# Performance work log

Hardware: AMD Instinct MI355X
Metric: run time of the kernel (lower is better)

Reference implementation:

```python
import jax, jax.numpy as jnp
import numpy as np

D = 512       # d_model
H = 8         # n_heads
HD = D // H   # head_dim = 64
BS = 64       # block_size
B = 1
S = 8192
NB = S // BS  # 128 blocks
THRESH = 0.3


def setup_inputs() -> dict:
    key = jax.random.key(0)
    ks = jax.random.split(key, 6)
    sc = 0.02
    return {
        "x": jax.random.normal(ks[0], (B, S, D), jnp.float32),
        "w_qkv": (jax.random.normal(ks[1], (D, 3 * D)) * sc).astype(jnp.float32),
        "b_qkv": jnp.zeros((3 * D,), jnp.float32),
        "w_out": (jax.random.normal(ks[2], (D, D)) * sc).astype(jnp.float32),
        "b_out": jnp.zeros((D,), jnp.float32),
        "w_r1": (jax.random.normal(ks[3], (D, 128)) * sc).astype(jnp.float32),
        "b_r1": jnp.zeros((128,), jnp.float32),
        "w_r2": (jax.random.normal(ks[4], (128, 1)) * sc).astype(jnp.float32),
        "b_r2": jnp.full((1,), 0.5, jnp.float32),  # sigmoid(~0.5)>0.3 -> non-degenerate mask
    }


def reference(x, w_qkv, b_qkv, w_out, b_out, w_r1, b_r1, w_r2, b_r2):
    Bx, Sx, Dx = x.shape
    qkv = (x @ w_qkv + b_qkv).reshape(Bx, Sx, 3, H, HD)
    q = jnp.transpose(qkv[:, :, 0], (0, 2, 1, 3))  # [B,H,S,HD]
    k = jnp.transpose(qkv[:, :, 1], (0, 2, 1, 3))
    v = jnp.transpose(qkv[:, :, 2], (0, 2, 1, 3))

    # --- router: per-block importance from mean-pooled q block (d_model features) ---
    qb = q.reshape(Bx, H, NB, BS, HD)
    rep = jnp.transpose(qb.mean(axis=3), (0, 2, 1, 3)).reshape(Bx, NB, Dx)  # [B,NB,D]
    imp = jax.nn.sigmoid(jax.nn.relu(rep @ w_r1 + b_r1) @ w_r2 + b_r2)[..., 0]  # [B,NB]
    keep = (imp.mean(axis=0) >= THRESH).astype(x.dtype)  # [NB], shared across batch (torch uses batch-mean)

    kb = k.reshape(Bx, H, NB, BS, HD)
    vb = v.reshape(Bx, H, NB, BS, HD)
    tri = jnp.triu(jnp.ones((BS, BS), bool), 1)  # strict upper triangle within diagonal block
    jidx = jnp.arange(NB)
    scale = 1.0 / np.sqrt(HD)

    def step(carry, i):
        q_i = jax.lax.dynamic_slice_in_dim(q, i * BS, BS, axis=2)        # [B,H,BSq,HD]
        s = jnp.einsum('bhqd,bhjkd->bhqjk', q_i, kb) * scale             # [B,H,BSq,NB,BSk]
        causal = (jidx == i)[None, :, None] & tri[:, None, :]            # [BSq,NB,BSk]
        s = jnp.where(causal[None, None], -jnp.inf, s)
        p = jax.nn.softmax(s, axis=-1)                                   # softmax PER key-block (as in torch loop)
        wj = keep * keep[i]                                              # block pair gate [NB]
        o = jnp.einsum('bhqjk,j,bhjkd->bhqd', p, wj, vb)                 # sum of gated per-block contributions
        return carry, o

    _, outs = jax.lax.scan(step, None, jnp.arange(NB))                   # [NB,B,H,BSq,HD]
    attn = jnp.transpose(outs, (1, 2, 0, 3, 4)).reshape(Bx, H, Sx, HD)
    attn = jnp.transpose(attn, (0, 2, 1, 3)).reshape(Bx, Sx, Dx)
    return attn @ w_out + b_out
```

## Files before the change

### kernel.cpp

```cpp
#include <hip/hip_runtime.h>

typedef unsigned short u16;
typedef unsigned int u32;
typedef __attribute__((ext_vector_type(8))) short short8;
typedef __attribute__((ext_vector_type(4))) short short4v;
typedef __attribute__((ext_vector_type(4))) float f32x4;
typedef __attribute__((ext_vector_type(4))) float float4v;
typedef __attribute__((ext_vector_type(2))) u32 u32x2;
typedef __attribute__((ext_vector_type(4))) u32 u32x4;

#define S_LEN 8192
#define NHEAD 8
#define NBLK  128
#define SCALE_C 0.18033688011112042f

#if __has_builtin(__builtin_amdgcn_permlane16_swap) && __has_builtin(__builtin_amdgcn_permlane32_swap)
#define HAVE_PLSWAP 1
#else
#define HAVE_PLSWAP 0
#endif

__device__ __forceinline__ u16 f2b(float f) {
    union { float f; unsigned u; } v; v.f = f;
    unsigned r = v.u + 0x7FFFu + ((v.u >> 16) & 1u);
    return (u16)(r >> 16);
}
__device__ __forceinline__ float b2f(u16 b) {
    union { float f; unsigned u; } v; v.u = ((unsigned)b) << 16; return v.f;
}
__device__ __forceinline__ u32 cvt_pk_bf16(float lo, float hi) {
    u32 r;
    asm("v_cvt_pk_bf16_f32 %0, %1, %2" : "=v"(r) : "v"(lo), "v"(hi));
    return r;
}
#if HAVE_PLSWAP
__device__ __forceinline__ void pl16swap(u32& a, u32& b) {
    u32x2 r = __builtin_amdgcn_permlane16_swap(a, b, false, false);
    a = r[0]; b = r[1];
}
__device__ __forceinline__ void pl32swap(u32& a, u32& b) {
    u32x2 r = __builtin_amdgcn_permlane32_swap(a, b, false, false);
    a = r[0]; b = r[1];
}
#endif
__device__ __forceinline__ int swz(int row, int colByte) {
    return row * 128 + (colByte ^ ((row & 7) << 4));
}

__global__ __launch_bounds__(256) void cvt_x_kernel(const float* __restrict__ x, u16* __restrict__ xb) {
    int idx = blockIdx.x * 256 + threadIdx.x;
    float4v v = *((const float4v*)x + idx);
    short4v o;
    #pragma unroll
    for (int r = 0; r < 4; ++r) o[r] = (short)f2b(v[r]);
    *((short4v*)xb + idx) = o;
}

__global__ __launch_bounds__(256) void cvt_T_kernel(const float* __restrict__ w, u16* __restrict__ wt, int C) {
    int idx = blockIdx.x * 256 + threadIdx.x;
    int r = idx & 511, cc = idx >> 9;
    wt[idx] = f2b(w[(size_t)r * C + cc]);
}

__device__ __forceinline__ void gemm128_core(const u16* __restrict__ A,
                                             const u16* __restrict__ Bt,
                                             int m0, int n0, char* As, char* Bs,
                                             f32x4 acc[4][4]) {
    const int tid = threadIdx.x;
    const int lane = tid & 63, wid = tid >> 6;
    const int q16 = lane >> 4, l16 = lane & 15;
    const int wm = wid >> 1, wn = wid & 1;
    #pragma unroll 1
    for (int kt = 0; kt < 8; ++kt) {
        const int k0 = kt * 64;
        short8 ra[4], rb[4];
        #pragma unroll
        for (int p = 0; p < 4; ++p) {
            int c = tid + p * 256;
            int row = c >> 3, col = c & 7;
            ra[p] = *(const short8*)(A  + (size_t)(m0 + row) * 512 + k0 + col * 8);
            rb[p] = *(const short8*)(Bt + (size_t)(n0 + row) * 512 + k0 + col * 8);
        }
        __syncthreads();
        #pragma unroll
        for (int p = 0; p < 4; ++p) {
            int c = tid + p * 256;
            int row = c >> 3, col = c & 7;
            *(short8*)(As + swz(row, col * 16)) = ra[p];
            *(short8*)(Bs + swz(row, col * 16)) = rb[p];
        }
        __syncthreads();
        #pragma unroll
        for (int kk = 0; kk < 2; ++kk) {
            short8 a[4], b[4];
            #pragma unroll
            for (int t = 0; t < 4; ++t) {
                int arow = wm * 64 + t * 16 + l16;
                a[t] = *(const short8*)(As + swz(arow, (kk * 32 + q16 * 8) * 2));
                int brow = wn * 64 + t * 16 + l16;
                b[t] = *(const short8*)(Bs + swz(brow, (kk * 32 + q16 * 8) * 2));
            }
            #pragma unroll
            for (int mt = 0; mt < 4; ++mt)
                #pragma unroll
                for (int nt = 0; nt < 4; ++nt)
                    acc[mt][nt] = __builtin_amdgcn_mfma_f32_16x16x32_bf16(a[mt], b[nt], acc[mt][nt], 0, 0, 0);
        }
    }
}

__global__ __launch_bounds__(256) void qkv_gemm(const u16* __restrict__ xb, const u16* __restrict__ wqkvT,
                                                const float* __restrict__ bqkv,
                                                u16* __restrict__ qb, u16* __restrict__ kb, u16* __restrict__ vt) {
    __shared__ char smem[32768];
    f32x4 acc[4][4];
    #pragma unroll
    for (int a = 0; a < 4; ++a)
        #pragma unroll
        for (int b = 0; b < 4; ++b) acc[a][b] = (f32x4){0.f, 0.f, 0.f, 0.f};
    const int m0 = blockIdx.x * 128, n0 = blockIdx.y * 128;
    gemm128_core(xb, wqkvT, m0, n0, smem, smem + 16384, acc);

    const int lane = threadIdx.x & 63, wid = threadIdx.x >> 6;
    const int q16 = lane >> 4, l16 = lane & 15;
    const int wm = wid >> 1, wn = wid & 1;
    #pragma unroll
    for (int mt = 0; mt < 4; ++mt) {
        #pragma unroll
        for (int nt = 0; nt < 4; ++nt) {
            int n = n0 + wn * 64 + nt * 16 + l16;
            float bias = bqkv[n];
            int t = n >> 9, h = (n >> 6) & 7, d = n & 63;
            int sb = m0 + wm * 64 + mt * 16 + q16 * 4;
            f32x4 v = acc[mt][nt];
            if (t == 2) {
                short4v pk;
                #pragma unroll
                for (int r = 0; r < 4; ++r) pk[r] = (short)f2b(v[r] + bias);
                *(short4v*)(vt + (size_t)(h * 64 + d) * S_LEN + sb) = pk;
            } else {
                u16* dst = (t == 0) ? qb : kb;
                float scale = (t == 0) ? SCALE_C : 1.0f;
                #pragma unroll
                for (int r = 0; r < 4; ++r)
                    dst[(size_t)(h * S_LEN + sb + r) * 64 + d] = f2b((v[r] + bias) * scale);
            }
        }
    }
}

__global__ __launch_bounds__(256) void out_gemm(const u16* __restrict__ a0, const u16* __restrict__ a1,
                                                const u16* __restrict__ wotT,
                                                const float* __restrict__ bout, float* __restrict__ out) {
    __shared__ char smem[32768];
    f32x4 acc[4][4];
    #pragma unroll
    for (int a = 0; a < 4; ++a)
        #pragma unroll
        for (int b = 0; b < 4; ++b) acc[a][b] = (f32x4){0.f, 0.f, 0.f, 0.f};
    const int m0 = blockIdx.x * 128, n0 = blockIdx.y * 128;
    gemm128_core(a0, wotT, m0, n0, smem, smem + 16384, acc);
    gemm128_core(a1, wotT, m0, n0, smem, smem + 16384, acc);

    const int lane = threadIdx.x & 63, wid = threadIdx.x >> 6;
    const int q16 = lane >> 4, l16 = lane & 15;
    const int wm = wid >> 1, wn = wid & 1;
    #pragma unroll
    for (int mt = 0; mt < 4; ++mt) {
        #pragma unroll
        for (int nt = 0; nt < 4; ++nt) {
            int n = n0 + wn * 64 + nt * 16 + l16;
            float bias = bout[n];
            int sb = m0 + wm * 64 + mt * 16 + q16 * 4;
            #pragma unroll
            for (int r = 0; r < 4; ++r)
                out[(size_t)(sb + r) * 512 + n] = acc[mt][nt][r] + bias;
        }
    }
}

__global__ __launch_bounds__(256) void router_kernel(const u16* __restrict__ qb,
                                                     const float* __restrict__ w_r1, const float* __restrict__ b_r1,
                                                     const float* __restrict__ w_r2, const float* __restrict__ b_r2,
                                                     float* __restrict__ keepf) {
    const int nb = blockIdx.x, tid = threadIdx.x;
    __shared__ float rep[512];
    __shared__ float h1[128];
    for (int dim = tid; dim < 512; dim += 256) {
        int h = dim >> 6, d = dim & 63;
        const u16* p = qb + (size_t)(h * S_LEN + nb * 64) * 64 + d;
        float s = 0.f;
        #pragma unroll 4
        for (int t = 0; t < 64; ++t) s += b2f(p[t * 64]);
        rep[dim] = s * (0.015625f / SCALE_C);
    }
    __syncthreads();
    if (tid < 128) {
        float a = b_r1[tid];
        for (int k = 0; k < 512; ++k) a += rep[k] * w_r1[k * 128 + tid];
        h1[tid] = fmaxf(a, 0.f);
    }
    __syncthreads();
    if (tid < 64) {
        float v = h1[tid] * w_r2[tid] + h1[tid + 64] * w_r2[tid + 64];
        #pragma unroll
        for (int off = 32; off; off >>= 1) v += __shfl_down(v, off);
        if (tid == 0) {
            float z = v + b_r2[0];
            keepf[nb] = (z >= -0.84729786f) ? 1.0f : 0.0f;
        }
    }
}

__global__ __launch_bounds__(256) void attn_kernel(const u16* __restrict__ qb, const u16* __restrict__ kb,
                                                   const u16* __restrict__ vt, const float* __restrict__ keepf,
                                                   u16* __restrict__ att0, u16* __restrict__ att1) {
    const int i = blockIdx.x, h = blockIdx.y, jh = blockIdx.z;
    const int j0 = jh * 64;
    u16* __restrict__ att = jh ? att1 : att0;
    const int tid = threadIdx.x, lane = tid & 63, wid = tid >> 6;
    const int q16 = lane >> 4, l16 = lane & 15;
    __shared__ char smem[32768];

    short8 bq0, bq1;
    {
        const u16* qrow = qb + (size_t)(h * S_LEN + i * 64 + wid * 16 + l16) * 64;
        bq0 = *(const short8*)(qrow + q16 * 8);
        bq1 = *(const short8*)(qrow + 32 + q16 * 8);
    }
    const float keep_i = keepf[i];
    const int qloc = wid * 16 + l16;

    f32x4 o[4];
    #pragma unroll
    for (int t = 0; t < 4; ++t) o[t] = (f32x4){0.f, 0.f, 0.f, 0.f};

    const int r0 = tid >> 3, col = tid & 7;
    const u16* kptr = kb + (size_t)(h * S_LEN + j0 * 64 + r0) * 64 + col * 8;
    const u16* vptr = vt + (size_t)(h * 64 + r0) * S_LEN + j0 * 64 + col * 8;
    const int swa = swz(r0, col * 16), swb = swz(r0 + 32, col * 16);
#if !HAVE_PLSWAP
    const bool sel_hi = (q16 >= 2);
    const int idx0 = (((2 * q16 + 0) & 3) * 16 + l16) * 4;
    const int idx1 = (((2 * q16 + 1) & 3) * 16 + l16) * 4;
#endif

    short8 kr0 = *(const short8*)kptr;
    short8 kr1 = *(const short8*)(kptr + 2048);
    short8 vr0 = *(const short8*)vptr;
    short8 vr1 = *(const short8*)(vptr + (size_t)32 * S_LEN);
    *(short8*)(smem + swa) = kr0;
    *(short8*)(smem + swb) = kr1;
    *(short8*)(smem + 8192 + swa) = vr0;
    *(short8*)(smem + 8192 + swb) = vr1;
    kr0 = *(const short8*)(kptr + 4096);
    kr1 = *(const short8*)(kptr + 4096 + 2048);
    vr0 = *(const short8*)(vptr + 64);
    vr1 = *(const short8*)(vptr + (size_t)32 * S_LEN + 64);
    __syncthreads();

    for (int jj = 0; jj < 64; ++jj) {
        char* Kc = smem + ((jj & 1) << 14);
        char* Vc = Kc + 8192;
        char* Kn = smem + (((jj + 1) & 1) << 14);
        char* Vn = Kn + 8192;
        if (jj < 63) {
            *(short8*)(Kn + swa) = kr0;
            *(short8*)(Kn + swb) = kr1;
            *(short8*)(Vn + swa) = vr0;
            *(short8*)(Vn + swb) = vr1;
        }
        if (jj < 62) {
            const u16* kn = kptr + (size_t)(jj + 2) * 4096;
            const u16* vn = vptr + (size_t)(jj + 2) * 64;
            kr0 = *(const short8*)kn;
            kr1 = *(const short8*)(kn + 2048);
            vr0 = *(const short8*)vn;
            vr1 = *(const short8*)(vn + (size_t)32 * S_LEN);
        }
        const float g = keep_i * keepf[j0 + jj];

        f32x4 s4[4];
        __builtin_amdgcn_s_setprio(1);
        #pragma unroll
        for (int n0 = 0; n0 < 4; ++n0) {
            short8 ka0 = *(const short8*)(Kc + swz(n0 * 16 + l16, q16 * 16));
            short8 ka1 = *(const short8*)(Kc + swz(n0 * 16 + l16, 64 + q16 * 16));
            f32x4 a = (f32x4){0.f, 0.f, 0.f, 0.f};
            a = __builtin_amdgcn_mfma_f32_16x16x32_bf16(ka0, bq0, a, 0, 0, 0);
            a = __builtin_amdgcn_mfma_f32_16x16x32_bf16(ka1, bq1, a, 0, 0, 0);
            s4[n0] = a;
        }
        __builtin_amdgcn_s_setprio(0);

        float pv[4][4];
        #pragma unroll
        for (int n0 = 0; n0 < 4; ++n0)
            #pragma unroll
            for (int r = 0; r < 4; ++r)
                pv[n0][r] = __builtin_amdgcn_exp2f(s4[n0][r]);
        if (j0 + jj == i) {
            #pragma unroll
            for (int n0 = 0; n0 < 4; ++n0)
                #pragma unroll
                for (int r = 0; r < 4; ++r)
                    if (n0 * 16 + q16 * 4 + r > qloc) pv[n0][r] = 0.f;
        }
        float sum = 0.f;
        #pragma unroll
        for (int n0 = 0; n0 < 4; ++n0)
            sum += (pv[n0][0] + pv[n0][1]) + (pv[n0][2] + pv[n0][3]);
#if HAVE_PLSWAP
        {
            u32 sa = __builtin_bit_cast(u32, sum), sb = sa;
            pl16swap(sa, sb);
            sum = __builtin_bit_cast(float, sa) + __builtin_bit_cast(float, sb);
            u32 sc = __builtin_bit_cast(u32, sum), sd = sc;
            pl32swap(sc, sd);
            sum = __builtin_bit_cast(float, sc) + __builtin_bit_cast(float, sd);
        }
#else
        sum += __shfl_xor(sum, 16);
        sum += __shfl_xor(sum, 32);
#endif
        const float rinv = g * __builtin_amdgcn_rcpf(sum);

        u32 dw[4][2];
        #pragma unroll
        for (int n0 = 0; n0 < 4; ++n0) {
            dw[n0][0] = cvt_pk_bf16(pv[n0][0] * rinv, pv[n0][1] * rinv);
            dw[n0][1] = cvt_pk_bf16(pv[n0][2] * rinv, pv[n0][3] * rinv);
        }
        short8 pb[2];
#if HAVE_PLSWAP
        #pragma unroll
        for (int kk = 0; kk < 2; ++kk) {
            u32 a0 = dw[2 * kk][0], b0 = dw[2 * kk + 1][0];
            pl32swap(a0, b0);
            pl16swap(a0, b0);
            u32 a1 = dw[2 * kk][1], b1 = dw[2 * kk + 1][1];
            pl32swap(a1, b1);
            pl16swap(a1, b1);
            u32x4 wv;
            wv[0] = a0; wv[1] = a1; wv[2] = b0; wv[3] = b1;
            pb[kk] = __builtin_bit_cast(short8, wv);
        }
#else
        {
            u32 pl0[4][2], pl1[4][2];
            #pragma unroll
            for (int n0 = 0; n0 < 4; ++n0)
                #pragma unroll
                for (int p = 0; p < 2; ++p) {
                    pl0[n0][p] = (u32)__builtin_amdgcn_ds_bpermute(idx0, (int)dw[n0][p]);
                    pl1[n0][p] = (u32)__builtin_amdgcn_ds_bpermute(idx1, (int)dw[n0][p]);
                }
            u32x4 bfa, bfb;
            bfa[0] = sel_hi ? pl0[1][0] : pl0[0][0];
            bfa[1] = sel_hi ? pl1[1][0] : pl1[0][0];
            bfa[2] = sel_hi ? pl0[1][1] : pl0[0][1];
            bfa[3] = sel_hi ? pl1[1][1] : pl1[0][1];
            bfb[0] = sel_hi ? pl0[3][0] : pl0[2][0];
            bfb[1] = sel_hi ? pl1[3][0] : pl1[2][0];
            bfb[2] = sel_hi ? pl0[3][1] : pl0[2][1];
            bfb[3] = sel_hi ? pl1[3][1] : pl1[2][1];
            pb[0] = __builtin_bit_cast(short8, bfa);
            pb[1] = __builtin_bit_cast(short8, bfb);
        }
#endif

        __builtin_amdgcn_s_setprio(1);
        #pragma unroll
        for (int dt = 0; dt < 4; ++dt) {
            short8 va0 = *(const short8*)(Vc + swz(dt * 16 + l16, q16 * 16));
            short8 va1 = *(const short8*)(Vc + swz(dt * 16 + l16, 64 + q16 * 16));
            o[dt] = __builtin_amdgcn_mfma_f32_16x16x32_bf16(va0, pb[0], o[dt], 0, 0, 0);
            o[dt] = __builtin_amdgcn_mfma_f32_16x16x32_bf16(va1, pb[1], o[dt], 0, 0, 0);
        }
        __builtin_amdgcn_s_setprio(0);

        __syncthreads();
    }

    u16* obase = att + (size_t)(i * 64 + wid * 16 + l16) * 512 + h * 64 + q16 * 4;
    #pragma unroll
    for (int dt = 0; dt < 4; ++dt) {
        u32x2 st;
        st[0] = cvt_pk_bf16(o[dt][0], o[dt][1]);
        st[1] = cvt_pk_bf16(o[dt][2], o[dt][3]);
        *(u32x2*)(obase + dt * 16) = st;
    }
}

static const size_t OFF_XB    = 0;
static const size_t OFF_WQKVT = OFF_XB    + (8u << 20);
static const size_t OFF_WOTT  = OFF_WQKVT + (2u << 20);
static const size_t OFF_QB    = OFF_WOTT  + (1u << 20);
static const size_t OFF_KB    = OFF_QB    + (8u << 20);
static const size_t OFF_VT    = OFF_KB    + (8u << 20);
static const size_t OFF_ATT   = OFF_VT    + (8u << 20);
static const size_t OFF_KEEP  = OFF_ATT   + (8u << 20);

extern "C" void kernel_launch(void* const* d_in, const int* in_sizes, int n_in,
                              void* d_out, int out_size, void* d_ws, size_t ws_size,
                              hipStream_t stream) {
    const float* x     = (const float*)d_in[0];
    const float* w_qkv = (const float*)d_in[1];
    const float* b_qkv = (const float*)d_in[2];
    const float* w_out = (const float*)d_in[3];
    const float* b_out = (const float*)d_in[4];
    const float* w_r1  = (const float*)d_in[5];
    const float* b_r1  = (const float*)d_in[6];
    const float* w_r2  = (const float*)d_in[7];
    const float* b_r2  = (const float*)d_in[8];
    float* out = (float*)d_out;
    char* ws = (char*)d_ws;
    u16* xb     = (u16*)(ws + OFF_XB);
    u16* wqkvT  = (u16*)(ws + OFF_WQKVT);
    u16* wotT   = (u16*)(ws + OFF_WOTT);
    u16* qb     = (u16*)(ws + OFF_QB);
    u16* kb     = (u16*)(ws + OFF_KB);
    u16* vt     = (u16*)(ws + OFF_VT);
    u16* attnb  = (u16*)(ws + OFF_ATT);
    u16* att1   = (u16*)(ws + OFF_XB);
    float* keepf = (float*)(ws + OFF_KEEP);

    cvt_x_kernel<<<4096, 256, 0, stream>>>(x, xb);
    cvt_T_kernel<<<3072, 256, 0, stream>>>(w_qkv, wqkvT, 1536);
    cvt_T_kernel<<<1024, 256, 0, stream>>>(w_out, wotT, 512);
    qkv_gemm<<<dim3(64, 12), 256, 0, stream>>>(xb, wqkvT, b_qkv, qb, kb, vt);
    router_kernel<<<128, 256, 0, stream>>>(qb, w_r1, b_r1, w_r2, b_r2, keepf);
    attn_kernel<<<dim3(128, 8, 2), 256, 0, stream>>>(qb, kb, vt, keepf, attnb, att1);
    out_gemm<<<dim3(64, 4), 256, 0, stream>>>(attnb, att1, wotT, b_out, out);
}
```

Before: 275.8 us.

## Double query rows per attention block and stage K/V via direct global-to-LDS loads

```diff
diff --git a/kernel.cpp b/kernel.cpp
--- a/kernel.cpp
+++ b/kernel.cpp
@@ -14,12 +14,6 @@
 #define NBLK  128
 #define SCALE_C 0.18033688011112042f
 
-#if __has_builtin(__builtin_amdgcn_permlane16_swap) && __has_builtin(__builtin_amdgcn_permlane32_swap)
-#define HAVE_PLSWAP 1
-#else
-#define HAVE_PLSWAP 0
-#endif
-
 __device__ __forceinline__ u16 f2b(float f) {
     union { float f; unsigned u; } v; v.f = f;
     unsigned r = v.u + 0x7FFFu + ((v.u >> 16) & 1u);
@@ -33,7 +27,6 @@
     asm("v_cvt_pk_bf16_f32 %0, %1, %2" : "=v"(r) : "v"(lo), "v"(hi));
     return r;
 }
-#if HAVE_PLSWAP
 __device__ __forceinline__ void pl16swap(u32& a, u32& b) {
     u32x2 r = __builtin_amdgcn_permlane16_swap(a, b, false, false);
     a = r[0]; b = r[1];
@@ -42,9 +35,13 @@
     u32x2 r = __builtin_amdgcn_permlane32_swap(a, b, false, false);
     a = r[0]; b = r[1];
 }
-#endif
 __device__ __forceinline__ int swz(int row, int colByte) {
     return row * 128 + (colByte ^ ((row & 7) << 4));
+}
+__device__ __forceinline__ void gload_lds(const void* g, void* l) {
+    __builtin_amdgcn_global_load_lds(
+        (const __attribute__((address_space(1))) void*)g,
+        (__attribute__((address_space(3))) void*)l, 16, 0, 0);
 }
 
 __global__ __launch_bounds__(256) void cvt_x_kernel(const float* __restrict__ x, u16* __restrict__ xb) {
@@ -73,21 +70,15 @@
     #pragma unroll 1
     for (int kt = 0; kt < 8; ++kt) {
         const int k0 = kt * 64;
-        short8 ra[4], rb[4];
+        __syncthreads();
         #pragma unroll
         for (int p = 0; p < 4; ++p) {
             int c = tid + p * 256;
-            int row = c >> 3, col = c & 7;
-            ra[p] = *(const short8*)(A  + (size_t)(m0 + row) * 512 + k0 + col * 8);
-            rb[p] = *(const short8*)(Bt + (size_t)(n0 + row) * 512 + k0 + col * 8);
-        }
-        __syncthreads();
-        #pragma unroll
-        for (int p = 0; p < 4; ++p) {
-            int c = tid + p * 256;
-            int row = c >> 3, col = c & 7;
-            *(short8*)(As + swz(row, col * 16)) = ra[p];
-            *(short8*)(Bs + swz(row, col * 16)) = rb[p];
+            int row = c >> 3, colp = (c & 7) ^ (row & 7);
+            char* dst = (char*)0 + (wid * 64 + p * 256) * 16;
+            gload_lds(A  + (size_t)(m0 + row) * 512 + k0 + colp * 8, As + (size_t)(wid * 64 + p * 256) * 16);
+            gload_lds(Bt + (size_t)(n0 + row) * 512 + k0 + colp * 8, Bs + (size_t)(wid * 64 + p * 256) * 16);
+            (void)dst;
         }
         __syncthreads();
         #pragma unroll
@@ -96,9 +87,9 @@
             #pragma unroll
             for (int t = 0; t < 4; ++t) {
                 int arow = wm * 64 + t * 16 + l16;
-                a[t] = *(const short8*)(As + swz(arow, (kk * 32 + q16 * 8) * 2));
+                a[t] = *(const short8*)(As + swz(arow, kk * 64 + q16 * 16));
                 int brow = wn * 64 + t * 16 + l16;
-                b[t] = *(const short8*)(Bs + swz(brow, (kk * 32 + q16 * 8) * 2));
+                b[t] = *(const short8*)(Bs + swz(brow, kk * 64 + q16 * 16));
             }
             #pragma unroll
             for (int mt = 0; mt < 4; ++mt)
@@ -212,9 +203,9 @@
     }
 }
 
-__global__ __launch_bounds__(256) void attn_kernel(const u16* __restrict__ qb, const u16* __restrict__ kb,
-                                                   const u16* __restrict__ vt, const float* __restrict__ keepf,
-                                                   u16* __restrict__ att0, u16* __restrict__ att1) {
+__global__ __launch_bounds__(256, 4) void attn_kernel(const u16* __restrict__ qb, const u16* __restrict__ kb,
+                                                      const u16* __restrict__ vt, const float* __restrict__ keepf,
+                                                      u16* __restrict__ att0, u16* __restrict__ att1) {
     const int i = blockIdx.x, h = blockIdx.y, jh = blockIdx.z;
     const int j0 = jh * 64;
     u16* __restrict__ att = jh ? att1 : att0;
@@ -222,173 +213,143 @@
     const int q16 = lane >> 4, l16 = lane & 15;
     __shared__ char smem[32768];
 
-    short8 bq0, bq1;
+    short8 bq[2][2];
+    #pragma unroll
+    for (int qh = 0; qh < 2; ++qh) {
+        const u16* qrow = qb + (size_t)(h * S_LEN + i * 128 + wid * 32 + qh * 16 + l16) * 64;
+        bq[qh][0] = *(const short8*)(qrow + q16 * 8);
+        bq[qh][1] = *(const short8*)(qrow + 32 + q16 * 8);
+    }
+    const int kq = i * 2 + (wid >> 1);
+    const float keep_i = keepf[kq];
+    const int qloc = (wid & 1) * 32 + l16;
+
+    f32x4 o[2][4];
+    #pragma unroll
+    for (int qh = 0; qh < 2; ++qh)
+        #pragma unroll
+        for (int t = 0; t < 4; ++t) o[qh][t] = (f32x4){0.f, 0.f, 0.f, 0.f};
+
+    const int rA = tid >> 3,          cA = (tid & 7) ^ (rA & 7);
+    const int rB = (tid + 256) >> 3,  cB = (tid & 7) ^ (rB & 7);
+    const u16* kb_h = kb + (size_t)h * S_LEN * 64;
+    const u16* vt_h = vt + (size_t)h * 64 * S_LEN;
+    const int ldw0 = wid * 1024, ldw1 = wid * 1024 + 4096;
+
     {
-        const u16* qrow = qb + (size_t)(h * S_LEN + i * 64 + wid * 16 + l16) * 64;
-        bq0 = *(const short8*)(qrow + q16 * 8);
-        bq1 = *(const short8*)(qrow + 32 + q16 * 8);
-    }
-    const float keep_i = keepf[i];
-    const int qloc = wid * 16 + l16;
-
-    f32x4 o[4];
-    #pragma unroll
-    for (int t = 0; t < 4; ++t) o[t] = (f32x4){0.f, 0.f, 0.f, 0.f};
-
-    const int r0 = tid >> 3, col = tid & 7;
-    const u16* kptr = kb + (size_t)(h * S_LEN + j0 * 64 + r0) * 64 + col * 8;
-    const u16* vptr = vt + (size_t)(h * 64 + r0) * S_LEN + j0 * 64 + col * 8;
-    const int swa = swz(r0, col * 16), swb = swz(r0 + 32, col * 16);
-#if !HAVE_PLSWAP
-    const bool sel_hi = (q16 >= 2);
-    const int idx0 = (((2 * q16 + 0) & 3) * 16 + l16) * 4;
-    const int idx1 = (((2 * q16 + 1) & 3) * 16 + l16) * 4;
-#endif
-
-    short8 kr0 = *(const short8*)kptr;
-    short8 kr1 = *(const short8*)(kptr + 2048);
-    short8 vr0 = *(const short8*)vptr;
-    short8 vr1 = *(const short8*)(vptr + (size_t)32 * S_LEN);
-    *(short8*)(smem + swa) = kr0;
-    *(short8*)(smem + swb) = kr1;
-    *(short8*)(smem + 8192 + swa) = vr0;
-    *(short8*)(smem + 8192 + swb) = vr1;
-    kr0 = *(const short8*)(kptr + 4096);
-    kr1 = *(const short8*)(kptr + 4096 + 2048);
-    vr0 = *(const short8*)(vptr + 64);
-    vr1 = *(const short8*)(vptr + (size_t)32 * S_LEN + 64);
+        char* base = smem;
+        gload_lds(kb_h + (size_t)(j0 * 64 + rA) * 64 + cA * 8, base + ldw0);
+        gload_lds(kb_h + (size_t)(j0 * 64 + rB) * 64 + cB * 8, base + ldw1);
+        gload_lds(vt_h + (size_t)rA * S_LEN + j0 * 64 + cA * 8, base + 8192 + ldw0);
+        gload_lds(vt_h + (size_t)rB * S_LEN + j0 * 64 + cB * 8, base + 8192 + ldw1);
+    }
     __syncthreads();
 
     for (int jj = 0; jj < 64; ++jj) {
+        const int j = j0 + jj;
         char* Kc = smem + ((jj & 1) << 14);
         char* Vc = Kc + 8192;
-        char* Kn = smem + (((jj + 1) & 1) << 14);
-        char* Vn = Kn + 8192;
         if (jj < 63) {
-            *(short8*)(Kn + swa) = kr0;
-            *(short8*)(Kn + swb) = kr1;
-            *(short8*)(Vn + swa) = vr0;
-            *(short8*)(Vn + swb) = vr1;
-        }
-        if (jj < 62) {
-            const u16* kn = kptr + (size_t)(jj + 2) * 4096;
-            const u16* vn = vptr + (size_t)(jj + 2) * 64;
-            kr0 = *(const short8*)kn;
-            kr1 = *(const short8*)(kn + 2048);
-            vr0 = *(const short8*)vn;
-            vr1 = *(const short8*)(vn + (size_t)32 * S_LEN);
-        }
-        const float g = keep_i * keepf[j0 + jj];
-
-        f32x4 s4[4];
+            char* Kn = smem + (((jj + 1) & 1) << 14);
+            gload_lds(kb_h + (size_t)((j + 1) * 64 + rA) * 64 + cA * 8, Kn + ldw0);
+            gload_lds(kb_h + (size_t)((j + 1) * 64 + rB) * 64 + cB * 8, Kn + ldw1);
+            gload_lds(vt_h + (size_t)rA * S_LEN + (j + 1) * 64 + cA * 8, Kn + 8192 + ldw0);
+            gload_lds(vt_h + (size_t)rB * S_LEN + (j + 1) * 64 + cB * 8, Kn + 8192 + ldw1);
+        }
+        const float gj = keep_i * keepf[j];
+
+        f32x4 s4[2][4];
         __builtin_amdgcn_s_setprio(1);
         #pragma unroll
         for (int n0 = 0; n0 < 4; ++n0) {
             short8 ka0 = *(const short8*)(Kc + swz(n0 * 16 + l16, q16 * 16));
             short8 ka1 = *(const short8*)(Kc + swz(n0 * 16 + l16, 64 + q16 * 16));
-            f32x4 a = (f32x4){0.f, 0.f, 0.f, 0.f};
-            a = __builtin_amdgcn_mfma_f32_16x16x32_bf16(ka0, bq0, a, 0, 0, 0);
-            a = __builtin_amdgcn_mfma_f32_16x16x32_bf16(ka1, bq1, a, 0, 0, 0);
-            s4[n0] = a;
+            #pragma unroll
+            for (int qh = 0; qh < 2; ++qh) {
+                f32x4 a = (f32x4){0.f, 0.f, 0.f, 0.f};
+                a = __builtin_amdgcn_mfma_f32_16x16x32_bf16(ka0, bq[qh][0], a, 0, 0, 0);
+                a = __builtin_amdgcn_mfma_f32_16x16x32_bf16(ka1, bq[qh][1], a, 0, 0, 0);
+                s4[qh][n0] = a;
+            }
         }
         __builtin_amdgcn_s_setprio(0);
 
-        float pv[4][4];
-        #pragma unroll
-        for (int n0 = 0; n0 < 4; ++n0)
-            #pragma unroll
-            for (int r = 0; r < 4; ++r)
-                pv[n0][r] = __builtin_amdgcn_exp2f(s4[n0][r]);
-        if (j0 + jj == i) {
+        short8 pb[2][2];
+        #pragma unroll
+        for (int qh = 0; qh < 2; ++qh) {
+            float pv[4][4];
             #pragma unroll
             for (int n0 = 0; n0 < 4; ++n0)
                 #pragma unroll
                 for (int r = 0; r < 4; ++r)
-                    if (n0 * 16 + q16 * 4 + r > qloc) pv[n0][r] = 0.f;
-        }
-        float sum = 0.f;
-        #pragma unroll
-        for (int n0 = 0; n0 < 4; ++n0)
-            sum += (pv[n0][0] + pv[n0][1]) + (pv[n0][2] + pv[n0][3]);
-#if HAVE_PLSWAP
-        {
-            u32 sa = __builtin_bit_cast(u32, sum), sb = sa;
-            pl16swap(sa, sb);
-            sum = __builtin_bit_cast(float, sa) + __builtin_bit_cast(float, sb);
-            u32 sc = __builtin_bit_cast(u32, sum), sd = sc;
-            pl32swap(sc, sd);
-            sum = __builtin_bit_cast(float, sc) + __builtin_bit_cast(float, sd);
-        }
-#else
-        sum += __shfl_xor(sum, 16);
-        sum += __shfl_xor(sum, 32);
-#endif
-        const float rinv = g * __builtin_amdgcn_rcpf(sum);
-
-        u32 dw[4][2];
-        #pragma unroll
-        for (int n0 = 0; n0 < 4; ++n0) {
-            dw[n0][0] = cvt_pk_bf16(pv[n0][0] * rinv, pv[n0][1] * rinv);
-            dw[n0][1] = cvt_pk_bf16(pv[n0][2] * rinv, pv[n0][3] * rinv);
-        }
-        short8 pb[2];
-#if HAVE_PLSWAP
-        #pragma unroll
-        for (int kk = 0; kk < 2; ++kk) {
-            u32 a0 = dw[2 * kk][0], b0 = dw[2 * kk + 1][0];
-            pl32swap(a0, b0);
-            pl16swap(a0, b0);
-            u32 a1 = dw[2 * kk][1], b1 = dw[2 * kk + 1][1];
-            pl32swap(a1, b1);
-            pl16swap(a1, b1);
-            u32x4 wv;
-            wv[0] = a0; wv[1] = a1; wv[2] = b0; wv[3] = b1;
-            pb[kk] = __builtin_bit_cast(short8, wv);
-        }
-#else
-        {
-            u32 pl0[4][2], pl1[4][2];
+                    pv[n0][r] = __builtin_amdgcn_exp2f(s4[qh][n0][r]);
+            if (j == kq) {
+                const int qthis = qloc + qh * 16;
+                #pragma unroll
+                for (int n0 = 0; n0 < 4; ++n0)
+                    #pragma unroll
+                    for (int r = 0; r < 4; ++r)
+                        if (n0 * 16 + q16 * 4 + r > qthis) pv[n0][r] = 0.f;
+            }
+            float sum = 0.f;
             #pragma unroll
             for (int n0 = 0; n0 < 4; ++n0)
-                #pragma unroll
-                for (int p = 0; p < 2; ++p) {
-                    pl0[n0][p] = (u32)__builtin_amdgcn_ds_bpermute(idx0, (int)dw[n0][p]);
-                    pl1[n0][p] = (u32)__builtin_amdgcn_ds_bpermute(idx1, (int)dw[n0][p]);
-                }
-            u32x4 bfa, bfb;
-            bfa[0] = sel_hi ? pl0[1][0] : pl0[0][0];
-            bfa[1] = sel_hi ? pl1[1][0] : pl1[0][0];
-            bfa[2] = sel_hi ? pl0[1][1] : pl0[0][1];
-            bfa[3] = sel_hi ? pl1[1][1] : pl1[0][1];
-            bfb[0] = sel_hi ? pl0[3][0] : pl0[2][0];
-            bfb[1] = sel_hi ? pl1[3][0] : pl1[2][0];
-            bfb[2] = sel_hi ? pl0[3][1] : pl0[2][1];
-            bfb[3] = sel_hi ? pl1[3][1] : pl1[2][1];
-            pb[0] = __builtin_bit_cast(short8, bfa);
-            pb[1] = __builtin_bit_cast(short8, bfb);
-        }
-#endif
+                sum += (pv[n0][0] + pv[n0][1]) + (pv[n0][2] + pv[n0][3]);
+            {
+                u32 sa = __builtin_bit_cast(u32, sum), sb = sa;
+                pl16swap(sa, sb);
+                sum = __builtin_bit_cast(float, sa) + __builtin_bit_cast(float, sb);
+                u32 sc = __builtin_bit_cast(u32, sum), sd = sc;
+                pl32swap(sc, sd);
+                sum = __builtin_bit_cast(float, sc) + __builtin_bit_cast(float, sd);
+            }
+            const float rinv = gj * __builtin_amdgcn_rcpf(sum);
+            u32 dw[4][2];
+            #pragma unroll
+            for (int n0 = 0; n0 < 4; ++n0) {
+                dw[n0][0] = cvt_pk_bf16(pv[n0][0] * rinv, pv[n0][1] * rinv);
+                dw[n0][1] = cvt_pk_bf16(pv[n0][2] * rinv, pv[n0][3] * rinv);
+            }
+            #pragma unroll
+            for (int kk = 0; kk < 2; ++kk) {
+                u32 a0 = dw[2 * kk][0], b0 = dw[2 * kk + 1][0];
+                pl32swap(a0, b0);
+                pl16swap(a0, b0);
+                u32 a1 = dw[2 * kk][1], b1 = dw[2 * kk + 1][1];
+                pl32swap(a1, b1);
+                pl16swap(a1, b1);
+                u32x4 wv;
+                wv[0] = a0; wv[1] = a1; wv[2] = b0; wv[3] = b1;
+                pb[qh][kk] = __builtin_bit_cast(short8, wv);
+            }
+        }
 
         __builtin_amdgcn_s_setprio(1);
         #pragma unroll
         for (int dt = 0; dt < 4; ++dt) {
             short8 va0 = *(const short8*)(Vc + swz(dt * 16 + l16, q16 * 16));
             short8 va1 = *(const short8*)(Vc + swz(dt * 16 + l16, 64 + q16 * 16));
-            o[dt] = __builtin_amdgcn_mfma_f32_16x16x32_bf16(va0, pb[0], o[dt], 0, 0, 0);
-            o[dt] = __builtin_amdgcn_mfma_f32_16x16x32_bf16(va1, pb[1], o[dt], 0, 0, 0);
+            #pragma unroll
+            for (int qh = 0; qh < 2; ++qh) {
+                o[qh][dt] = __builtin_amdgcn_mfma_f32_16x16x32_bf16(va0, pb[qh][0], o[qh][dt], 0, 0, 0);
+                o[qh][dt] = __builtin_amdgcn_mfma_f32_16x16x32_bf16(va1, pb[qh][1], o[qh][dt], 0, 0, 0);
+            }
         }
         __builtin_amdgcn_s_setprio(0);
 
         __syncthreads();
     }
 
-    u16* obase = att + (size_t)(i * 64 + wid * 16 + l16) * 512 + h * 64 + q16 * 4;
-    #pragma unroll
-    for (int dt = 0; dt < 4; ++dt) {
-        u32x2 st;
-        st[0] = cvt_pk_bf16(o[dt][0], o[dt][1]);
-        st[1] = cvt_pk_bf16(o[dt][2], o[dt][3]);
-        *(u32x2*)(obase + dt * 16) = st;
+    #pragma unroll
+    for (int qh = 0; qh < 2; ++qh) {
+        u16* obase = att + (size_t)(i * 128 + wid * 32 + qh * 16 + l16) * 512 + h * 64 + q16 * 4;
+        #pragma unroll
+        for (int dt = 0; dt < 4; ++dt) {
+            u32x2 st;
+            st[0] = cvt_pk_bf16(o[qh][dt][0], o[qh][dt][1]);
+            st[1] = cvt_pk_bf16(o[qh][dt][2], o[qh][dt][3]);
+            *(u32x2*)(obase + dt * 16) = st;
+        }
     }
 }
 
@@ -430,6 +391,6 @@
     cvt_T_kernel<<<1024, 256, 0, stream>>>(w_out, wotT, 512);
     qkv_gemm<<<dim3(64, 12), 256, 0, stream>>>(xb, wqkvT, b_qkv, qb, kb, vt);
     router_kernel<<<128, 256, 0, stream>>>(qb, w_r1, b_r1, w_r2, b_r2, keepf);
-    attn_kernel<<<dim3(128, 8, 2), 256, 0, stream>>>(qb, kb, vt, keepf, attnb, att1);
+    attn_kernel<<<dim3(64, 8, 2), 256, 0, stream>>>(qb, kb, vt, keepf, attnb, att1);
     out_gemm<<<dim3(64, 4), 256, 0, stream>>>(attnb, att1, wotT, b_out, out);
 }
```

Measured after the change: 243.5 us. 1.13x faster.
